# Optimization experiments

Measured on AMD Instinct MI355X. Metric: run time of the kernel, lower is better.

The kernel has to match this reference:

```python
import jax, jax.numpy as jnp
import numpy as np

B, S, FDIM = 8, 512, 512
SUB = 4
DIM = FDIM // SUB            # 128 (reformer model dim)
HEADS, LOCAL_HEADS = 8, 2
LSH_HEADS = HEADS - LOCAL_HEADS
DH = 64                      # dim_head
INNER = HEADS * DH           # 512
BUCKET = 64
N_HASHES = 4
MEM = 128                    # num_mem_kv
DEPTH = 2                    # cfg.selfatn.num_layers
T = S * SUB + MEM            # 2176 internal seq (tokens + mem kv)
NB = T // BUCKET             # 34 buckets (even)
WINDOW = BUCKET * 2          # local attention window = 128
SELF_VAL = -5e4              # TOKEN_SELF_ATTN_VALUE
NEG = -1e9


def _ln(x, g, b, eps=1e-5):
    m = jnp.mean(x, -1, keepdims=True)
    v = jnp.mean((x - m) ** 2, -1, keepdims=True)
    return (x - m) * jax.lax.rsqrt(v + eps) * g + b


def _pos_encoding(s, d):
    pos = jnp.arange(s, dtype=jnp.float32)[:, None]
    i = jnp.arange(d, dtype=jnp.float32)
    div = 10000.0 ** (2.0 * i / d)
    pe = jnp.zeros((s, d), jnp.float32)
    pe = pe.at[:, 0::2].set(jnp.sin(pos / div[0::2]))
    pe = pe.at[:, 1::2].set(jnp.cos(pos / div[1::2]))
    return pe


def _l2norm(x, eps=1e-12):
    n = jnp.linalg.norm(x, axis=-1, keepdims=True)
    return x / jnp.maximum(n, eps)


def _lsh_attn(qk, v, rot):
    # qk, v: [Bh, T, DH]; rot: [DH, N_HASHES, NB//2] random rotations
    Bh, t, d = qk.shape
    rv = jnp.einsum('btf,fhi->bhti', qk, rot)
    rv = jnp.concatenate([rv, -rv], axis=-1)               # [Bh, nh, t, NB]
    buckets = jnp.argmax(rv, axis=-1)
    buckets = buckets + (jnp.arange(N_HASHES) * NB)[None, :, None]
    buckets = buckets.reshape(Bh, N_HASHES * t)
    ticker = jnp.arange(N_HASHES * t) % t
    key = buckets * t + ticker                             # sort by (bucket, pos)
    perm = jnp.argsort(key, axis=-1)                       # stable
    undo = jnp.argsort(perm, axis=-1)
    st = perm % t                                          # source positions
    sqk = jnp.take_along_axis(qk, st[..., None], axis=1)
    sv = jnp.take_along_axis(v, st[..., None], axis=1)
    C = N_HASHES * NB
    bq_t = st.reshape(Bh, C, BUCKET)
    bq = sqk.reshape(Bh, C, BUCKET, d)
    bv = sv.reshape(Bh, C, BUCKET, d)
    bk = _l2norm(bq)                                       # shared-QK: normalized keys
    look = lambda x: jnp.concatenate([x, jnp.roll(x, 1, axis=1)], axis=2)
    bk, bv, bkv_t = look(bk), look(bv), look(bq_t)
    dots = jnp.einsum('bcie,bcje->bcij', bq, bk) * (d ** -0.5)
    dots = jnp.where(bq_t[..., None] < bkv_t[:, :, None, :], NEG, dots)      # causal
    dots = jnp.where(bq_t[..., None] == bkv_t[:, :, None, :], SELF_VAL, dots)  # self
    lse = jax.nn.logsumexp(dots, axis=-1, keepdims=True)
    bo = jnp.einsum('bcij,bcje->bcie', jnp.exp(dots - lse), bv)
    so = bo.reshape(Bh, N_HASHES * t, d)
    slog = lse.reshape(Bh, N_HASHES * t)
    o = jnp.take_along_axis(so, undo[..., None], axis=1).reshape(Bh, N_HASHES, t, d)
    logits = jnp.take_along_axis(slog, undo, axis=1).reshape(Bh, N_HASHES, t, 1)
    w = jnp.exp(logits - jax.nn.logsumexp(logits, axis=1, keepdims=True))
    return (o * w).sum(axis=1)


def _local_attn(q, v):
    # shared-QK causal local attention, look_backward=1; q, v: [Bh, T, DH]
    Bh, t, d = q.shape
    W = t // WINDOW
    k = _l2norm(q)
    bq = q.reshape(Bh, W, WINDOW, d)
    bk = k.reshape(Bh, W, WINDOW, d)
    bv = v.reshape(Bh, W, WINDOW, d)
    tt = jnp.arange(t).reshape(W, WINDOW)
    prev = lambda x: jnp.concatenate([jnp.zeros_like(x[:, :1]), x[:, :-1]], axis=1)
    bk2 = jnp.concatenate([prev(bk), bk], axis=2)          # [Bh, W, 2W, d]
    bv2 = jnp.concatenate([prev(bv), bv], axis=2)
    tprev = jnp.concatenate([jnp.full((1, WINDOW), -1), tt[:-1]], axis=0)
    bkv_t = jnp.concatenate([tprev, tt], axis=1)           # [W, 2*WINDOW]
    dots = jnp.einsum('bwie,bwje->bwij', bq, bk2) * (d ** -0.5)
    dots = jnp.where(tt[:, :, None] == bkv_t[:, None, :], SELF_VAL, dots)
    dots = jnp.where(tt[:, :, None] < bkv_t[:, None, :], NEG, dots)
    dots = jnp.where((bkv_t == -1)[:, None, :], NEG, dots)
    attn = jax.nn.softmax(dots, axis=-1)
    return jnp.einsum('bwij,bwje->bwie', attn, bv2).reshape(Bh, t, d)


def _attn_layer(x, w_qk, w_v, mem_kv, w_out, b_out, rot):
    b, t0, _ = x.shape
    mem = jnp.broadcast_to(mem_kv, (b, MEM, DIM))
    xm = jnp.concatenate([x, mem], axis=1)                 # [b, T, DIM]
    qk = (xm @ w_qk).reshape(b, T, HEADS, DH).transpose(0, 2, 1, 3)
    v = (xm @ w_v).reshape(b, T, HEADS, DH).transpose(0, 2, 1, 3)
    merge = lambda a: a.reshape(-1, T, DH)
    out_loc = _local_attn(merge(qk[:, :LOCAL_HEADS]), merge(v[:, :LOCAL_HEADS]))
    out_lsh = _lsh_attn(merge(qk[:, LOCAL_HEADS:]), merge(v[:, LOCAL_HEADS:]), rot)
    out = jnp.concatenate([out_loc.reshape(b, LOCAL_HEADS, T, DH),
                           out_lsh.reshape(b, LSH_HEADS, T, DH)], axis=1)
    out = out.transpose(0, 2, 1, 3).reshape(b, T, INNER)
    return out[:, :t0] @ w_out + b_out


def setup_inputs() -> dict:
    key = jax.random.key(0)
    ks = jax.random.split(key, 20)
    std = 0.01  # init_network truncated-normal std
    p = lambda k, sh: std * jax.random.truncated_normal(k, -2.0, 2.0, sh, jnp.float32)
    return {
        'features': jax.random.normal(ks[0], (B, S, FDIM), jnp.float32),
        'w_qk': p(ks[1], (DEPTH, DIM, INNER)),
        'w_v': p(ks[2], (DEPTH, DIM, INNER)),
        'mem_kv': p(ks[3], (DEPTH, MEM, DIM)),
        'w_out': p(ks[4], (DEPTH, INNER, DIM)),
        'b_out': p(ks[5], (DEPTH, DIM)),
        'ln1_g': jnp.ones((DEPTH, DIM), jnp.float32),
        'ln1_b': jnp.zeros((DEPTH, DIM), jnp.float32),
        'ff_w1': p(ks[6], (DEPTH, DIM, 4 * DIM)),
        'ff_b1': p(ks[7], (DEPTH, 4 * DIM)),
        'ff_w2': p(ks[8], (DEPTH, 4 * DIM, DIM)),
        'ff_b2': p(ks[9], (DEPTH, DIM)),
        'ln2_g': jnp.ones((DEPTH, DIM), jnp.float32),
        'ln2_b': jnp.zeros((DEPTH, DIM), jnp.float32),
        'lnf_g': jnp.ones((DIM,), jnp.float32),
        'lnf_b': jnp.zeros((DIM,), jnp.float32),
        'rotations': jax.random.normal(ks[10], (DEPTH, DH, N_HASHES, NB // 2), jnp.float32),
    }


def reference(features, w_qk, w_v, mem_kv, w_out, b_out, ln1_g, ln1_b,
              ff_w1, ff_b1, ff_w2, ff_b2, ln2_g, ln2_b, lnf_g, lnf_b, rotations):
    b, s, fd = features.shape
    x = features + _pos_encoding(s, fd)                    # PositionalEncoding
    x = x.reshape(b, s * SUB, fd // SUB)                   # subspace split
    # reversible Reformer blocks: y1 = x1 + attn(ln(x2)); y2 = x2 + ff(ln(y1))
    x1, x2 = x, x
    for i in range(DEPTH):
        a_in = _ln(x2, ln1_g[i], ln1_b[i])
        y1 = x1 + _attn_layer(a_in, w_qk[i], w_v[i], mem_kv[i], w_out[i], b_out[i], rotations[i])
        g_in = _ln(y1, ln2_g[i], ln2_b[i])
        h = jax.nn.gelu(g_in @ ff_w1[i] + ff_b1[i], approximate=False)
        y2 = x2 + (h @ ff_w2[i] + ff_b2[i])
        x1, x2 = y1, y2
    x = 0.5 * (x1 + x2)                                    # mean of the two streams
    x = _ln(x, lnf_g, lnf_b)                               # final norm
    x = x.reshape(b, s, fd)                                # merge subspaces back
    return x.mean(axis=1)                                  # AvgPool
```

## Files before the change

kernel.cpp:

```cpp
#include <hip/hip_runtime.h>
#include <math.h>

#define NB_ 34
#define NEGV  (-1e9f)
#define SELFV (-5e4f)

typedef __attribute__((ext_vector_type(8))) short short8;
typedef __attribute__((ext_vector_type(4))) float floatx4;

__device__ __forceinline__ unsigned short f2bf(float f) {
  unsigned int u = __float_as_uint(f);
  u += 0x7fffu + ((u >> 16) & 1u);
  return (unsigned short)(u >> 16);
}
__device__ __forceinline__ float bflo(unsigned int u) { return __uint_as_float(u << 16); }
__device__ __forceinline__ float bfhi(unsigned int u) { return __uint_as_float(u & 0xffff0000u); }

__device__ __forceinline__ void load_row64_bf(const unsigned short* __restrict__ p, float* q) {
#pragma unroll
  for (int k = 0; k < 8; ++k) {
    uint4 u = ((const uint4*)p)[k];
    q[8*k+0]=bflo(u.x); q[8*k+1]=bfhi(u.x);
    q[8*k+2]=bflo(u.y); q[8*k+3]=bfhi(u.y);
    q[8*k+4]=bflo(u.z); q[8*k+5]=bfhi(u.z);
    q[8*k+6]=bflo(u.w); q[8*k+7]=bfhi(u.w);
  }
}


__global__ void pos_kernel(const float* __restrict__ feat, float* __restrict__ x1,
                           float* __restrict__ x2) {
  int idx = blockIdx.x*256 + threadIdx.x;
  int d = idx & 127, t = (idx >> 7) & 2047, b = idx >> 18;
  int s = t >> 2, c = ((t & 3) << 7) | d;
  float div = powf(10000.0f, (float)c * (1.0f/256.0f));
  float arg = (float)s / div;
  float pe = (c & 1) ? cosf(arg) : sinf(arg);
  float val = feat[((size_t)b*512 + s)*512 + c] + pe;
  x1[idx] = val; x2[idx] = val;
}

__global__ __launch_bounds__(256) void ln_kernel(
    const float* __restrict__ in, const float* __restrict__ in2,
    const float* __restrict__ g, const float* __restrict__ bta,
    void* __restrict__ out, int rows, int ou, int oa, int obf) {
  int wid = threadIdx.x >> 6, lane = threadIdx.x & 63;
  int row = blockIdx.x*4 + wid;
  if (row >= rows) return;
  float2 x = ((const float2*)(in + (size_t)row*128))[lane];
  if (in2) {
    float2 y = ((const float2*)(in2 + (size_t)row*128))[lane];
    x.x = 0.5f*(x.x + y.x); x.y = 0.5f*(x.y + y.y);
  }
  float s = x.x + x.y;
#pragma unroll
  for (int m = 1; m < 64; m <<= 1) s += __shfl_xor(s, m, 64);
  float mean = s * (1.0f/128.0f);
  float dx = x.x - mean, dy = x.y - mean;
  float v = dx*dx + dy*dy;
#pragma unroll
  for (int m = 1; m < 64; m <<= 1) v += __shfl_xor(v, m, 64);
  float inv = 1.0f / sqrtf(v*(1.0f/128.0f) + 1e-5f);
  int orow = (ou == oa) ? row : (row/ou)*oa + (row%ou);
  float2 gg = ((const float2*)g)[lane];
  float2 bb = ((const float2*)bta)[lane];
  float ox = dx*inv*gg.x + bb.x, oy = dy*inv*gg.y + bb.y;
  if (obf) {
    ((unsigned int*)out)[(size_t)orow*64 + lane] =
        (unsigned int)f2bf(ox) | ((unsigned int)f2bf(oy) << 16);
  } else {
    float2 o; o.x = ox; o.y = oy;
    ((float2*)((float*)out + (size_t)orow*128))[lane] = o;
  }
}

__global__ void memfill_kernel(const float* __restrict__ mem,
                               unsigned short* __restrict__ xmb) {
  int idx = blockIdx.x*256 + threadIdx.x;
  int d = idx & 127, r = (idx >> 7) & 127, b = idx >> 14;
  xmb[((size_t)b*2176 + 2048 + r)*128 + d] = f2bf(mem[(r << 7) | d]);
}

__global__ void wconv_kernel(const float* __restrict__ w, unsigned short* __restrict__ wt,
                             int K, int N) {
  int idx = blockIdx.x*256 + threadIdx.x;
  int k = idx % K, n = idx / K;
  wt[idx] = f2bf(w[(size_t)k*N + n]);
}

__global__ __launch_bounds__(256) void gemm_bf16(
    const unsigned short* __restrict__ A, const unsigned short* __restrict__ Wt,
    const float* __restrict__ bias, const float* __restrict__ resid,
    float* __restrict__ C, unsigned short* __restrict__ Cb,
    int M, int N, int K, int au, int aa, int act) {
  __shared__ __align__(16) unsigned short As[64*40];
  __shared__ __align__(16) unsigned short Bs[64*40];
  int tid = threadIdx.x;
  int wid = tid >> 6, l15 = tid & 15, quad = (tid & 63) >> 4;
  int mb = blockIdx.y, nb = blockIdx.x;
  int r = tid >> 2, cc = (tid & 3)*8;
  int rg = mb*64 + r;
  int rp = (au == aa) ? rg : (rg/au)*aa + (rg%au);
  const unsigned short* arow = A + (size_t)rp*K + cc;
  const unsigned short* brow = Wt + (size_t)(nb*64 + r)*K + cc;
  floatx4 acc[4];
#pragma unroll
  for (int mt = 0; mt < 4; ++mt) acc[mt] = (floatx4){0.f,0.f,0.f,0.f};
  for (int k0 = 0; k0 < K; k0 += 32) {
    *(short8*)&As[r*40 + cc] = *(const short8*)(arow + k0);
    *(short8*)&Bs[r*40 + cc] = *(const short8*)(brow + k0);
    __syncthreads();
    short8 bfr = *(const short8*)&Bs[(wid*16 + l15)*40 + quad*8];
#pragma unroll
    for (int mt = 0; mt < 4; ++mt) {
      short8 afr = *(const short8*)&As[(mt*16 + l15)*40 + quad*8];
      acc[mt] = __builtin_amdgcn_mfma_f32_16x16x32_bf16(afr, bfr, acc[mt], 0, 0, 0);
    }
    __syncthreads();
  }
  int n = nb*64 + wid*16 + l15;
  float bi = bias ? bias[n] : 0.f;
#pragma unroll
  for (int mt = 0; mt < 4; ++mt) {
#pragma unroll
    for (int rr = 0; rr < 4; ++rr) {
      int m = mb*64 + mt*16 + quad*4 + rr;
      float val = acc[mt][rr] + bi;
      if (act) val = 0.5f*val*(1.0f + erff(val*0.70710678118654752f));
      if (resid) val += resid[(size_t)m*N + n];
      if (Cb) Cb[(size_t)m*N + n] = f2bf(val);
      else    C[(size_t)m*N + n] = val;
    }
  }
}

__global__ __launch_bounds__(256) void gemm_qv(
    const unsigned short* __restrict__ A, const unsigned short* __restrict__ Wt,
    unsigned short* __restrict__ Q, unsigned short* __restrict__ V) {
  __shared__ __align__(16) unsigned short As[64*40];
  __shared__ __align__(16) unsigned short Bs[64*40];
  int tid = threadIdx.x;
  int wid = tid >> 6, l15 = tid & 15, quad = (tid & 63) >> 4;
  int mb = blockIdx.y, nb = blockIdx.x;
  int r = tid >> 2, cc = (tid & 3)*8;
  const unsigned short* arow = A + (size_t)(mb*64 + r)*128 + cc;
  const unsigned short* brow = Wt + (size_t)(nb*64 + r)*128 + cc;
  floatx4 acc[4];
#pragma unroll
  for (int mt = 0; mt < 4; ++mt) acc[mt] = (floatx4){0.f,0.f,0.f,0.f};
#pragma unroll
  for (int k0 = 0; k0 < 128; k0 += 32) {
    *(short8*)&As[r*40 + cc] = *(const short8*)(arow + k0);
    *(short8*)&Bs[r*40 + cc] = *(const short8*)(brow + k0);
    __syncthreads();
    short8 bfr = *(const short8*)&Bs[(wid*16 + l15)*40 + quad*8];
#pragma unroll
    for (int mt = 0; mt < 4; ++mt) {
      short8 afr = *(const short8*)&As[(mt*16 + l15)*40 + quad*8];
      acc[mt] = __builtin_amdgcn_mfma_f32_16x16x32_bf16(afr, bfr, acc[mt], 0, 0, 0);
    }
    __syncthreads();
  }
  int n = nb*64 + wid*16 + l15;
#pragma unroll
  for (int mt = 0; mt < 4; ++mt) {
#pragma unroll
    for (int rr = 0; rr < 4; ++rr) {
      int m = mb*64 + mt*16 + quad*4 + rr;
      unsigned short bv = f2bf(acc[mt][rr]);
      if (n < 512) Q[(size_t)m*512 + n] = bv;
      else         V[(size_t)m*512 + (n - 512)] = bv;
    }
  }
}

__global__ __launch_bounds__(256) void norm_kernel(const unsigned short* __restrict__ qkb,
                                                   float* __restrict__ nrm) {
  int idx = blockIdx.x*256 + threadIdx.x;
  int head = idx & 7, row = idx >> 3;
  const uint4* src = (const uint4*)(qkb + (size_t)row*512 + head*64);
  float ss = 0.f;
#pragma unroll
  for (int k = 0; k < 8; ++k) {
    uint4 u = src[k];
    ss += bflo(u.x)*bflo(u.x) + bfhi(u.x)*bfhi(u.x)
        + bflo(u.y)*bflo(u.y) + bfhi(u.y)*bfhi(u.y)
        + bflo(u.z)*bflo(u.z) + bfhi(u.z)*bfhi(u.z)
        + bflo(u.w)*bflo(u.w) + bfhi(u.w)*bfhi(u.w);
  }
  int b = row / 2176, t = row % 2176;
  nrm[((size_t)b*8 + head)*2176 + t] = 1.0f / fmaxf(sqrtf(ss), 1e-12f);
}

__global__ __launch_bounds__(128) void local_attn_mfma(
    const unsigned short* __restrict__ qkb, const unsigned short* __restrict__ vbb,
    const float* __restrict__ nrm,
    unsigned short* __restrict__ opart, float* __restrict__ lpart) {
  __shared__ __align__(16) unsigned short qq[128*72];
  __shared__ __align__(16) unsigned short kk[128*72];
  __shared__ __align__(16) unsigned short vt[64*136];
  __shared__ __align__(16) unsigned short ptile[2][16*136];
  __shared__ float invn[128];

  int blk = blockIdx.x;
  int part = blk & 1;
  int bw = blk >> 1;
  int bh = bw / 17, w = bw % 17;
  int b = bh >> 1, coloff = (bh & 1)*64;
  int tid = threadIdx.x;
  int t_qbase = w*128;

  unsigned short* obase = opart + (size_t)(part*16 + bh)*2176*64;
  float* lbase = lpart + (size_t)(part*16 + bh)*2176;

  if (part == 0 && w == 0) {
    uint4 z = {0,0,0,0};
    uint4* orow = (uint4*)(obase + (size_t)tid*64);
#pragma unroll
    for (int j = 0; j < 8; ++j) orow[j] = z;
    lbase[tid] = -1e9f;
    return;
  }

  int tkbase = part ? t_qbase : (t_qbase - 128);
  const float* nrmh = nrm + ((size_t)b*8 + (bh & 1))*2176;
  invn[tid] = nrmh[tkbase + tid];

  {
    const unsigned short* qr = qkb + ((size_t)(b*2176 + t_qbase + tid)*512 + coloff);
#pragma unroll
    for (int k = 0; k < 8; ++k) *(uint4*)&qq[tid*72 + k*8] = ((const uint4*)qr)[k];
  }
  if (part == 0) {
    const unsigned short* qr = qkb + ((size_t)(b*2176 + t_qbase - 128 + tid)*512 + coloff);
#pragma unroll
    for (int k = 0; k < 8; ++k) *(uint4*)&kk[tid*72 + k*8] = ((const uint4*)qr)[k];
  }
  if (tid < 64) {
    const unsigned short* vrA = vbb + ((size_t)(b*2176 + tkbase + 2*tid)*512 + coloff);
    const unsigned short* vrB = vrA + 512;
    unsigned int* vt32 = (unsigned int*)vt;
#pragma unroll
    for (int k = 0; k < 8; ++k) {
      uint4 ua = ((const uint4*)vrA)[k];
      uint4 uc = ((const uint4*)vrB)[k];
      const unsigned short* pa = (const unsigned short*)&ua;
      const unsigned short* pc = (const unsigned short*)&uc;
#pragma unroll
      for (int j = 0; j < 8; ++j) {
        int d = 8*k + j;
        vt32[d*68 + tid] = (unsigned int)pa[j] | ((unsigned int)pc[j] << 16);
      }
    }
  }
  __syncthreads();

  int wid = tid >> 6, l15 = tid & 15, quad = (tid & 63) >> 4;
  const unsigned short* keyrows = part ? qq : kk;
  float sm8[8];
#pragma unroll
  for (int nt = 0; nt < 8; ++nt) sm8[nt] = invn[nt*16 + l15] * 0.125f;
  int qrow0 = wid*64;
  unsigned short* pt = &ptile[wid][0];

#pragma unroll
  for (int mt = 0; mt < 4; ++mt) {
    floatx4 acc[8];
#pragma unroll
    for (int nt = 0; nt < 8; ++nt) acc[nt] = (floatx4){0.f,0.f,0.f,0.f};
#pragma unroll
    for (int ks = 0; ks < 2; ++ks) {
      short8 afr = *(const short8*)&qq[(qrow0 + mt*16 + l15)*72 + ks*32 + quad*8];
#pragma unroll
      for (int nt = 0; nt < 8; ++nt) {
        short8 bfr = *(const short8*)&keyrows[(nt*16 + l15)*72 + ks*32 + quad*8];
        acc[nt] = __builtin_amdgcn_mfma_f32_16x16x32_bf16(afr, bfr, acc[nt], 0, 0, 0);
      }
    }
    float invl[4];
#pragma unroll
    for (int r = 0; r < 4; ++r) {
      int row = qrow0 + mt*16 + quad*4 + r;
      int t_q = t_qbase + row;
      float sv[8]; float mx = -INFINITY;
#pragma unroll
      for (int nt = 0; nt < 8; ++nt) {
        float sc = acc[nt][r] * sm8[nt];
        int t_k = tkbase + nt*16 + l15;
        sc = (t_k > t_q) ? NEGV : (t_k == t_q ? SELFV : sc);
        sv[nt] = sc; mx = fmaxf(mx, sc);
      }
#pragma unroll
      for (int m2 = 1; m2 < 16; m2 <<= 1) mx = fmaxf(mx, __shfl_xor(mx, m2, 64));
      float l = 0.f;
#pragma unroll
      for (int nt = 0; nt < 8; ++nt) { float pe = expf(sv[nt] - mx); sv[nt] = pe; l += pe; }
#pragma unroll
      for (int m2 = 1; m2 < 16; m2 <<= 1) l += __shfl_xor(l, m2, 64);
      invl[r] = 1.0f / l;
#pragma unroll
      for (int nt = 0; nt < 8; ++nt)
        pt[(quad*4 + r)*136 + nt*16 + l15] = f2bf(sv[nt]);
      if (l15 == 0) lbase[t_q] = mx + logf(l);
    }
#pragma unroll
    for (int nt = 0; nt < 4; ++nt) {
      floatx4 po = (floatx4){0.f,0.f,0.f,0.f};
#pragma unroll
      for (int ks = 0; ks < 4; ++ks) {
        short8 afr = *(const short8*)&pt[l15*136 + ks*32 + quad*8];
        short8 bfr = *(const short8*)&vt[(nt*16 + l15)*136 + ks*32 + quad*8];
        po = __builtin_amdgcn_mfma_f32_16x16x32_bf16(afr, bfr, po, 0, 0, 0);
      }
      int d = nt*16 + l15;
#pragma unroll
      for (int r = 0; r < 4; ++r) {
        int t_q = t_qbase + qrow0 + mt*16 + quad*4 + r;
        obase[(size_t)t_q*64 + d] = f2bf(po[r] * invl[r]);
      }
    }
  }
}

__global__ void local_comb(const unsigned short* __restrict__ opart,
                           const float* __restrict__ lpart,
                           unsigned short* __restrict__ aob) {
  int idx = blockIdx.x*256 + threadIdx.x;
  if (idx >= 16*2176*8) return;
  int f8 = idx & 7;
  int p  = (idx >> 3) % 2176;
  int bh = idx / (8*2176);
  float lg0 = lpart[(size_t)bh*2176 + p];
  float lg1 = lpart[(size_t)(16 + bh)*2176 + p];
  float m = fmaxf(lg0, lg1);
  float e0 = expf(lg0 - m), e1 = expf(lg1 - m);
  float inv = 1.0f / (e0 + e1);
  float w0 = e0*inv, w1 = e1*inv;
  uint4 u0 = ((const uint4*)(opart + ((size_t)bh*2176 + p)*64))[f8];
  uint4 u1 = ((const uint4*)(opart + ((size_t)(16 + bh)*2176 + p)*64))[f8];
  uint4 o;
  o.x = (unsigned int)f2bf(w0*bflo(u0.x) + w1*bflo(u1.x)) |
        ((unsigned int)f2bf(w0*bfhi(u0.x) + w1*bfhi(u1.x)) << 16);
  o.y = (unsigned int)f2bf(w0*bflo(u0.y) + w1*bflo(u1.y)) |
        ((unsigned int)f2bf(w0*bfhi(u0.y) + w1*bfhi(u1.y)) << 16);
  o.z = (unsigned int)f2bf(w0*bflo(u0.z) + w1*bflo(u1.z)) |
        ((unsigned int)f2bf(w0*bfhi(u0.z) + w1*bfhi(u1.z)) << 16);
  o.w = (unsigned int)f2bf(w0*bflo(u0.w) + w1*bflo(u1.w)) |
        ((unsigned int)f2bf(w0*bfhi(u0.w) + w1*bfhi(u1.w)) << 16);
  int b = bh >> 1;
  ((uint4*)(aob + ((size_t)(b*2176 + p)*512 + (bh & 1)*64 + f8*8)))[0] = o;
}

__global__ __launch_bounds__(256) void hash_kernel(
    const unsigned short* __restrict__ qkb, const float* __restrict__ rot,
    int* __restrict__ bucket) {
  __shared__ float rl[64*68];
  for (int l = threadIdx.x; l < 4352; l += 256) rl[l] = rot[l];
  __syncthreads();
  int idx = blockIdx.x*256 + threadIdx.x;
  int p = idx % 2176, bh = idx / 2176;
  int b = bh / 6, hh = bh % 6;
  float q[64];
  load_row64_bf(qkb + ((size_t)(b*2176 + p)*512 + (2+hh)*64), q);
  for (int h = 0; h < 4; ++h) {
    float rv[17];
#pragma unroll
    for (int k = 0; k < 17; ++k) rv[k] = 0.f;
    for (int d = 0; d < 64; ++d) {
      float qd = q[d];
      const float* rp = &rl[d*68 + h*17];
#pragma unroll
      for (int k = 0; k < 17; ++k) rv[k] = fmaf(qd, rp[k], rv[k]);
    }
    float best = rv[0]; int bi = 0;
#pragma unroll
    for (int k = 1; k < 34; ++k) {
      float val = (k < 17) ? rv[k] : -rv[k-17];
      if (val > best) { best = val; bi = k; }
    }
    bucket[(size_t)(bh*4 + h)*2176 + p] = bi;
  }
}

__global__ __launch_bounds__(256) void sort_kernel(const int* __restrict__ bucket,
                                                   int* __restrict__ st) {
  __shared__ int sb[2176];
  __shared__ int cnt[NB_*256];
  __shared__ int csum[256];
  int tid = threadIdx.x;
  int bhh = blockIdx.x;
  const int* bin = bucket + (size_t)bhh*2176;
  for (int p = tid; p < 2176; p += 256) sb[p] = bin[p];
#pragma unroll
  for (int j = 0; j < NB_; ++j) cnt[j*256 + tid] = 0;
  __syncthreads();
  int s0 = tid*9;
  int e = s0 + 9; if (e > 2176) e = 2176;
  for (int p = s0; p < e; ++p) cnt[sb[p]*256 + tid] += 1;
  __syncthreads();
  {
    int sum = 0;
    int base0 = tid*NB_;
#pragma unroll
    for (int j = 0; j < NB_; ++j) {
      int v = cnt[base0 + j];
      cnt[base0 + j] = sum;
      sum += v;
    }
    csum[tid] = sum;
  }
  __syncthreads();
  for (int off = 1; off < 256; off <<= 1) {
    int v = (tid >= off) ? csum[tid - off] : 0;
    __syncthreads();
    csum[tid] += v;
    __syncthreads();
  }
  {
    int base = tid ? csum[tid-1] : 0;
    int base0 = tid*NB_;
#pragma unroll
    for (int j = 0; j < NB_; ++j) cnt[base0 + j] += base;
  }
  __syncthreads();
  int bh = bhh >> 2, h = bhh & 3;
  int* outp = st + (size_t)bh*8704 + h*2176;
  for (int p = s0; p < e; ++p) {
    int bk = sb[p];
    int r = cnt[bk*256 + tid]++;
    outp[r] = p;
  }
}

__global__ __launch_bounds__(128) void lsh_attn_mfma(
    const unsigned short* __restrict__ qkb, const unsigned short* __restrict__ vbb,
    const float* __restrict__ nrm, const int* __restrict__ st,
    unsigned short* __restrict__ o_all, float* __restrict__ logits) {
  __shared__ __align__(16) unsigned short qq[192*72];
  __shared__ __align__(16) unsigned short vt[64*200];
  __shared__ __align__(16) unsigned short ptile[2][16*136];
  __shared__ int   tkl[192];
  __shared__ float invn[192];

  int blk = blockIdx.x;
  int bh = blk / 68, pair = blk % 68;
  int c0 = pair*2;
  int b = bh / 6, coloff = (2 + bh % 6)*64;
  int tid = threadIdx.x;
  const float* nrmh = nrm + ((size_t)b*8 + 2 + bh % 6)*2176;

#pragma unroll
  for (int rr = 0; rr < 2; ++rr) {
    if (rr == 1 && tid >= 64) break;
    int r = (rr == 0) ? tid : 128 + tid;
    int cr = c0 - 1 + (r >> 6); if (cr < 0) cr += 136;
    int p = st[(size_t)bh*8704 + cr*64 + (r & 63)];
    tkl[r] = p;
    invn[r] = nrmh[p];
    const unsigned short* qr = qkb + ((size_t)(b*2176 + p)*512 + coloff);
#pragma unroll
    for (int k = 0; k < 8; ++k) *(uint4*)&qq[r*72 + k*8] = ((const uint4*)qr)[k];
  }
  if (tid < 96) {
    int r0 = 2*tid, r1 = r0 + 1;
    int cr0 = c0 - 1 + (r0 >> 6); if (cr0 < 0) cr0 += 136;
    int cr1 = c0 - 1 + (r1 >> 6); if (cr1 < 0) cr1 += 136;
    int p0 = st[(size_t)bh*8704 + cr0*64 + (r0 & 63)];
    int p1 = st[(size_t)bh*8704 + cr1*64 + (r1 & 63)];
    const unsigned short* a = vbb + ((size_t)(b*2176 + p0)*512 + coloff);
    const unsigned short* c = vbb + ((size_t)(b*2176 + p1)*512 + coloff);
    unsigned int* vt32 = (unsigned int*)vt;
#pragma unroll
    for (int k = 0; k < 8; ++k) {
      uint4 ua = ((const uint4*)a)[k];
      uint4 uc = ((const uint4*)c)[k];
      const unsigned short* pa = (const unsigned short*)&ua;
      const unsigned short* pc = (const unsigned short*)&uc;
#pragma unroll
      for (int j = 0; j < 8; ++j) {
        int d = 8*k + j;
        vt32[d*100 + tid] = (unsigned int)pa[j] | ((unsigned int)pc[j] << 16);
      }
    }
  }
  __syncthreads();

  int wid = tid >> 6, l15 = tid & 15, quad = (tid & 63) >> 4;
  int kbase = wid*64, qbase = 64 + wid*64;
  int c = c0 + wid;
  int h = c / NB_;
  float sm8[8]; int tk8[8];
#pragma unroll
  for (int nt = 0; nt < 8; ++nt) {
    int kr = kbase + nt*16 + l15;
    sm8[nt] = invn[kr] * 0.125f;
    tk8[nt] = tkl[kr];
  }
  float* logrow = logits + (size_t)(bh*4 + h)*2176;
  unsigned short* obase = o_all + (size_t)(bh*4 + h)*2176*64;
  unsigned short* pt = &ptile[wid][0];

#pragma unroll
  for (int mt = 0; mt < 4; ++mt) {
    floatx4 acc[8];
#pragma unroll
    for (int nt = 0; nt < 8; ++nt) acc[nt] = (floatx4){0.f,0.f,0.f,0.f};
#pragma unroll
    for (int ks = 0; ks < 2; ++ks) {
      short8 afr = *(const short8*)&qq[(qbase + mt*16 + l15)*72 + ks*32 + quad*8];
#pragma unroll
      for (int nt = 0; nt < 8; ++nt) {
        short8 bfr = *(const short8*)&qq[(kbase + nt*16 + l15)*72 + ks*32 + quad*8];
        acc[nt] = __builtin_amdgcn_mfma_f32_16x16x32_bf16(afr, bfr, acc[nt], 0, 0, 0);
      }
    }
    float invl[4];
#pragma unroll
    for (int r = 0; r < 4; ++r) {
      int t_q = tkl[qbase + mt*16 + quad*4 + r];
      float sv8[8]; float mx = -INFINITY;
#pragma unroll
      for (int nt = 0; nt < 8; ++nt) {
        float sc = acc[nt][r] * sm8[nt];
        int t_k = tk8[nt];
        sc = (t_k > t_q) ? NEGV : (t_k == t_q ? SELFV : sc);
        sv8[nt] = sc; mx = fmaxf(mx, sc);
      }
#pragma unroll
      for (int m2 = 1; m2 < 16; m2 <<= 1) mx = fmaxf(mx, __shfl_xor(mx, m2, 64));
      float l = 0.f;
#pragma unroll
      for (int nt = 0; nt < 8; ++nt) { float pe = expf(sv8[nt] - mx); sv8[nt] = pe; l += pe; }
#pragma unroll
      for (int m2 = 1; m2 < 16; m2 <<= 1) l += __shfl_xor(l, m2, 64);
      invl[r] = 1.0f / l;
#pragma unroll
      for (int nt = 0; nt < 8; ++nt)
        pt[(quad*4 + r)*136 + nt*16 + l15] = f2bf(sv8[nt]);
      if (l15 == 0) logrow[t_q] = mx + logf(l);
    }
#pragma unroll
    for (int nt = 0; nt < 4; ++nt) {
      floatx4 po = (floatx4){0.f,0.f,0.f,0.f};
#pragma unroll
      for (int ks = 0; ks < 4; ++ks) {
        short8 afr = *(const short8*)&pt[l15*136 + ks*32 + quad*8];
        short8 bfr = *(const short8*)&vt[(nt*16 + l15)*200 + kbase + ks*32 + quad*8];
        po = __builtin_amdgcn_mfma_f32_16x16x32_bf16(afr, bfr, po, 0, 0, 0);
      }
      int d = nt*16 + l15;
#pragma unroll
      for (int r = 0; r < 4; ++r) {
        int p_q = tkl[qbase + mt*16 + quad*4 + r];
        obase[(size_t)p_q*64 + d] = f2bf(po[r] * invl[r]);
      }
    }
  }
}

__global__ void comb_kernel(const unsigned short* __restrict__ o_all,
                            const float* __restrict__ logits,
                            unsigned short* __restrict__ aob) {
  int idx = blockIdx.x*256 + threadIdx.x;
  int f8 = idx & 7;
  int p  = (idx >> 3) % 2176;
  int bh = idx / (8*2176);
  float lg0 = logits[(size_t)(bh*4+0)*2176 + p];
  float lg1 = logits[(size_t)(bh*4+1)*2176 + p];
  float lg2 = logits[(size_t)(bh*4+2)*2176 + p];
  float lg3 = logits[(size_t)(bh*4+3)*2176 + p];
  float m = fmaxf(fmaxf(lg0, lg1), fmaxf(lg2, lg3));
  float e0 = expf(lg0-m), e1 = expf(lg1-m), e2 = expf(lg2-m), e3 = expf(lg3-m);
  float inv = 1.0f / (e0+e1+e2+e3);
  float wh[4] = {e0*inv, e1*inv, e2*inv, e3*inv};
  float o[8];
#pragma unroll
  for (int d = 0; d < 8; ++d) o[d] = 0.f;
#pragma unroll
  for (int h = 0; h < 4; ++h) {
    float wg = wh[h];
    uint4 u = ((const uint4*)(o_all + ((size_t)(bh*4+h)*2176 + p)*64))[f8];
    o[0] = fmaf(wg, bflo(u.x), o[0]); o[1] = fmaf(wg, bfhi(u.x), o[1]);
    o[2] = fmaf(wg, bflo(u.y), o[2]); o[3] = fmaf(wg, bfhi(u.y), o[3]);
    o[4] = fmaf(wg, bflo(u.z), o[4]); o[5] = fmaf(wg, bfhi(u.z), o[5]);
    o[6] = fmaf(wg, bflo(u.w), o[6]); o[7] = fmaf(wg, bfhi(u.w), o[7]);
  }
  int b = bh / 6, hh = bh % 6;
  uint4 u;
  u.x = (unsigned int)f2bf(o[0]) | ((unsigned int)f2bf(o[1]) << 16);
  u.y = (unsigned int)f2bf(o[2]) | ((unsigned int)f2bf(o[3]) << 16);
  u.z = (unsigned int)f2bf(o[4]) | ((unsigned int)f2bf(o[5]) << 16);
  u.w = (unsigned int)f2bf(o[6]) | ((unsigned int)f2bf(o[7]) << 16);
  ((uint4*)(aob + ((size_t)(b*2176 + p)*512 + (2+hh)*64 + f8*8)))[0] = u;
}

__global__ __launch_bounds__(256) void pool_kernel(const float* __restrict__ xln,
                                                   float* __restrict__ out) {
  int o = blockIdx.x*4 + (threadIdx.x >> 6);
  int lane = threadIdx.x & 63;
  int c = o & 511, b = o >> 9;
  int sub = c >> 7, d = c & 127;
  const float* p = xln + ((size_t)b*2048 + sub)*128 + d;
  float s = 0.f;
#pragma unroll
  for (int j = 0; j < 8; ++j) s += p[(size_t)(lane + 64*j)*512];
#pragma unroll
  for (int m = 1; m < 64; m <<= 1) s += __shfl_xor(s, m, 64);
  if (lane == 0) out[o] = s * (1.0f/512.0f);
}

#define OFF_X1    0ull
#define OFF_X2    2097152ull
#define OFF_XM    4194304ull
#define OFF_XMB   6422528ull
#define OFF_QKB   7536640ull
#define OFF_VB    16449536ull
#define OFF_AOB   25362432ull
#define OFF_OALL  29818880ull
#define OFF_LOG   43188224ull
#define OFF_BKT   43606016ull
#define OFF_ST    44023808ull
#define OFF_WTB   44441600ull
#define OFF_NRM   44769280ull
#define WS_FLOATS 44908544ull

extern "C" void kernel_launch(void* const* d_in, const int* in_sizes, int n_in,
                              void* d_out, int out_size, void* d_ws, size_t ws_size,
                              hipStream_t stream) {
  (void)in_sizes; (void)n_in; (void)out_size;
  if (ws_size < WS_FLOATS * 4ull) return;

  const float* feat  = (const float*)d_in[0];
  const float* w_qk  = (const float*)d_in[1];
  const float* w_v   = (const float*)d_in[2];
  const float* memkv = (const float*)d_in[3];
  const float* w_out = (const float*)d_in[4];
  const float* b_out = (const float*)d_in[5];
  const float* ln1g  = (const float*)d_in[6];
  const float* ln1b  = (const float*)d_in[7];
  const float* ffw1  = (const float*)d_in[8];
  const float* ffb1  = (const float*)d_in[9];
  const float* ffw2  = (const float*)d_in[10];
  const float* ffb2  = (const float*)d_in[11];
  const float* ln2g  = (const float*)d_in[12];
  const float* ln2b  = (const float*)d_in[13];
  const float* lnfg  = (const float*)d_in[14];
  const float* lnfb  = (const float*)d_in[15];
  const float* rots  = (const float*)d_in[16];

  float* ws = (float*)d_ws;
  float* x1   = ws + OFF_X1;
  float* x2   = ws + OFF_X2;
  float* xm   = ws + OFF_XM;
  unsigned short* xmb = (unsigned short*)(ws + OFF_XMB);
  unsigned short* qkb = (unsigned short*)(ws + OFF_QKB);
  unsigned short* vbb = (unsigned short*)(ws + OFF_VB);
  unsigned short* aob = (unsigned short*)(ws + OFF_AOB);
  unsigned short* hb  = (unsigned short*)(ws + OFF_AOB);
  unsigned short* oall = (unsigned short*)(ws + OFF_OALL);
  unsigned short* opart = (unsigned short*)(ws + OFF_OALL);
  float* lpart = ws + OFF_OALL + 2228224ull;
  float* logi = ws + OFF_LOG;
  int*   bkt  = (int*)(ws + OFF_BKT);
  int*   st   = (int*)(ws + OFF_ST);
  unsigned short* wtb = (unsigned short*)(ws + OFF_WTB);
  float* nrm  = ws + OFF_NRM;
  float* outp = (float*)d_out;

  pos_kernel<<<8192, 256, 0, stream>>>(feat, x1, x2);

  for (int i = 0; i < 2; ++i) {
    wconv_kernel<<<256, 256, 0, stream>>>(w_qk + i*65536, wtb + (i*5+0)*65536, 128, 512);
    wconv_kernel<<<256, 256, 0, stream>>>(w_v  + i*65536, wtb + (i*5+1)*65536, 128, 512);
    wconv_kernel<<<256, 256, 0, stream>>>(w_out+ i*65536, wtb + (i*5+2)*65536, 512, 128);
    wconv_kernel<<<256, 256, 0, stream>>>(ffw1 + i*65536, wtb + (i*5+3)*65536, 128, 512);
    wconv_kernel<<<256, 256, 0, stream>>>(ffw2 + i*65536, wtb + (i*5+4)*65536, 512, 128);
  }

  for (int i = 0; i < 2; ++i) {
    const unsigned short* Wqv = wtb + (i*5+0)*65536;
    const unsigned short* Wo  = wtb + (i*5+2)*65536;
    const unsigned short* W1  = wtb + (i*5+3)*65536;
    const unsigned short* W2  = wtb + (i*5+4)*65536;

    ln_kernel<<<4096, 256, 0, stream>>>(x2, nullptr, ln1g + i*128, ln1b + i*128,
                                        xmb, 16384, 2048, 2176, 1);
    memfill_kernel<<<512, 256, 0, stream>>>(memkv + i*16384, xmb);

    gemm_qv<<<dim3(16, 272), 256, 0, stream>>>(xmb, Wqv, qkb, vbb);
    norm_kernel<<<544, 256, 0, stream>>>(qkb, nrm);

    local_attn_mfma<<<544, 128, 0, stream>>>(qkb, vbb, nrm, opart, lpart);
    local_comb<<<1088, 256, 0, stream>>>(opart, lpart, aob);

    hash_kernel<<<408, 256, 0, stream>>>(qkb, rots + i*4352, bkt);
    sort_kernel<<<192, 256, 0, stream>>>(bkt, st);
    lsh_attn_mfma<<<3264, 128, 0, stream>>>(qkb, vbb, nrm, st, oall, logi);
    comb_kernel<<<3264, 256, 0, stream>>>(oall, logi, aob);

    gemm_bf16<<<dim3(2, 256), 256, 0, stream>>>(aob, Wo, b_out + i*128, x1, x1, nullptr,
                                                16384, 128, 512, 2048, 2176, 0);
    ln_kernel<<<4096, 256, 0, stream>>>(x1, nullptr, ln2g + i*128, ln2b + i*128,
                                        xmb, 16384, 1, 1, 1);
    gemm_bf16<<<dim3(8, 256), 256, 0, stream>>>(xmb, W1, ffb1 + i*512, nullptr, nullptr, hb,
                                                16384, 512, 128, 1, 1, 1);
    gemm_bf16<<<dim3(2, 256), 256, 0, stream>>>(hb, W2, ffb2 + i*128, x2, x2, nullptr,
                                                16384, 128, 512, 1, 1, 0);
  }

  ln_kernel<<<4096, 256, 0, stream>>>(x1, x2, lnfg, lnfb, xm, 16384, 1, 1, 0);
  pool_kernel<<<1024, 256, 0, stream>>>(xm, outp);
}
```

Measured before the change: 763.3 us.

## Fuse local and LSH attention launches, combine kernels, memfill, and weight conversion

Merges the local-window and LSH attention kernels into one launch that branches on block index, and merges their two combine kernels into one. The memory-kv fill is folded into the first layernorm launch, and the ten weight-conversion launches become one. The local partial outputs get their own workspace region so both attention paths can run at the same time. This cuts launch count and lets the two attention workloads fill the GPU together, but it uses a larger shared-memory allocation per block, which may lower occupancy for the local path.

After: 704.3 us. 1.08x faster.

```diff
diff --git a/kernel.cpp b/kernel.cpp
--- a/kernel.cpp
+++ b/kernel.cpp
@@ -43,10 +43,20 @@
 __global__ __launch_bounds__(256) void ln_kernel(
     const float* __restrict__ in, const float* __restrict__ in2,
     const float* __restrict__ g, const float* __restrict__ bta,
-    void* __restrict__ out, int rows, int ou, int oa, int obf) {
+    void* __restrict__ out, int rows, int ou, int oa, int obf,
+    const float* __restrict__ mem, int memrows) {
   int wid = threadIdx.x >> 6, lane = threadIdx.x & 63;
   int row = blockIdx.x*4 + wid;
-  if (row >= rows) return;
+  if (row >= rows) {
+    int mr = row - rows;
+    if (!mem || mr >= memrows) return;
+    int bb = mr >> 7, r = mr & 127;
+    int orow2 = bb*2176 + 2048 + r;
+    float2 mv = ((const float2*)(mem + (size_t)r*128))[lane];
+    ((unsigned int*)out)[(size_t)orow2*64 + lane] =
+        (unsigned int)f2bf(mv.x) | ((unsigned int)f2bf(mv.y) << 16);
+    return;
+  }
   float2 x = ((const float2*)(in + (size_t)row*128))[lane];
   if (in2) {
     float2 y = ((const float2*)(in2 + (size_t)row*128))[lane];
@@ -74,18 +84,24 @@
   }
 }
 
-__global__ void memfill_kernel(const float* __restrict__ mem,
-                               unsigned short* __restrict__ xmb) {
+__global__ void wconv_all(const float* __restrict__ w_qk, const float* __restrict__ w_v,
+                          const float* __restrict__ w_out, const float* __restrict__ ffw1,
+                          const float* __restrict__ ffw2, unsigned short* __restrict__ wt) {
   int idx = blockIdx.x*256 + threadIdx.x;
-  int d = idx & 127, r = (idx >> 7) & 127, b = idx >> 14;
-  xmb[((size_t)b*2176 + 2048 + r)*128 + d] = f2bf(mem[(r << 7) | d]);
-}
-
-__global__ void wconv_kernel(const float* __restrict__ w, unsigned short* __restrict__ wt,
-                             int K, int N) {
-  int idx = blockIdx.x*256 + threadIdx.x;
-  int k = idx % K, n = idx / K;
-  wt[idx] = f2bf(w[(size_t)k*N + n]);
+  int m = idx >> 16, j = idx & 65535;
+  int i = m / 5, t = m % 5;
+  const float* src; int K;
+  switch (t) {
+    case 0: src = w_qk; K = 128; break;
+    case 1: src = w_v;  K = 128; break;
+    case 2: src = w_out;K = 512; break;
+    case 3: src = ffw1; K = 128; break;
+    default:src = ffw2; K = 512; break;
+  }
+  src += (size_t)i*65536;
+  int N = 65536 / K;
+  int k = j % K, n = j / K;
+  wt[(size_t)m*65536 + j] = f2bf(src[(size_t)k*N + n]);
 }
 
 __global__ __launch_bounds__(256) void gemm_bf16(
@@ -192,163 +208,262 @@
   nrm[((size_t)b*8 + head)*2176 + t] = 1.0f / fmaxf(sqrtf(ss), 1e-12f);
 }
 
-__global__ __launch_bounds__(128) void local_attn_mfma(
+__global__ __launch_bounds__(128) void fused_attn(
     const unsigned short* __restrict__ qkb, const unsigned short* __restrict__ vbb,
-    const float* __restrict__ nrm,
+    const float* __restrict__ nrm, const int* __restrict__ st,
+    unsigned short* __restrict__ o_all, float* __restrict__ logits,
     unsigned short* __restrict__ opart, float* __restrict__ lpart) {
-  __shared__ __align__(16) unsigned short qq[128*72];
-  __shared__ __align__(16) unsigned short kk[128*72];
-  __shared__ __align__(16) unsigned short vt[64*136];
-  __shared__ __align__(16) unsigned short ptile[2][16*136];
-  __shared__ float invn[128];
-
-  int blk = blockIdx.x;
-  int part = blk & 1;
-  int bw = blk >> 1;
-  int bh = bw / 17, w = bw % 17;
-  int b = bh >> 1, coloff = (bh & 1)*64;
+  __shared__ __align__(16) unsigned char shraw[63488];
   int tid = threadIdx.x;
-  int t_qbase = w*128;
-
-  unsigned short* obase = opart + (size_t)(part*16 + bh)*2176*64;
-  float* lbase = lpart + (size_t)(part*16 + bh)*2176;
-
-  if (part == 0 && w == 0) {
-    uint4 z = {0,0,0,0};
-    uint4* orow = (uint4*)(obase + (size_t)tid*64);
-#pragma unroll
-    for (int j = 0; j < 8; ++j) orow[j] = z;
-    lbase[tid] = -1e9f;
+
+  if (blockIdx.x < 3264) {
+    unsigned short* qq = (unsigned short*)shraw;
+    unsigned short* vt = (unsigned short*)(shraw + 27648);
+    unsigned short* ptile = (unsigned short*)(shraw + 53248);
+    int*   tkl  = (int*)(shraw + 61952);
+    float* invn = (float*)(shraw + 62720);
+
+    int blk = blockIdx.x;
+    int bh = blk / 68, pair = blk % 68;
+    int c0 = pair*2;
+    int b = bh / 6, coloff = (2 + bh % 6)*64;
+    const float* nrmh = nrm + ((size_t)b*8 + 2 + bh % 6)*2176;
+
+#pragma unroll
+    for (int rr = 0; rr < 2; ++rr) {
+      if (rr == 1 && tid >= 64) break;
+      int r = (rr == 0) ? tid : 128 + tid;
+      int cr = c0 - 1 + (r >> 6); if (cr < 0) cr += 136;
+      int p = st[(size_t)bh*8704 + cr*64 + (r & 63)];
+      tkl[r] = p;
+      invn[r] = nrmh[p];
+      const unsigned short* qr = qkb + ((size_t)(b*2176 + p)*512 + coloff);
+#pragma unroll
+      for (int k = 0; k < 8; ++k) *(uint4*)&qq[r*72 + k*8] = ((const uint4*)qr)[k];
+    }
+    if (tid < 96) {
+      int r0 = 2*tid, r1 = r0 + 1;
+      int cr0 = c0 - 1 + (r0 >> 6); if (cr0 < 0) cr0 += 136;
+      int cr1 = c0 - 1 + (r1 >> 6); if (cr1 < 0) cr1 += 136;
+      int p0 = st[(size_t)bh*8704 + cr0*64 + (r0 & 63)];
+      int p1 = st[(size_t)bh*8704 + cr1*64 + (r1 & 63)];
+      const unsigned short* a = vbb + ((size_t)(b*2176 + p0)*512 + coloff);
+      const unsigned short* c = vbb + ((size_t)(b*2176 + p1)*512 + coloff);
+      unsigned int* vt32 = (unsigned int*)vt;
+#pragma unroll
+      for (int k = 0; k < 8; ++k) {
+        uint4 ua = ((const uint4*)a)[k];
+        uint4 uc = ((const uint4*)c)[k];
+        const unsigned short* pa = (const unsigned short*)&ua;
+        const unsigned short* pc = (const unsigned short*)&uc;
+#pragma unroll
+        for (int j = 0; j < 8; ++j) {
+          int d = 8*k + j;
+          vt32[d*100 + tid] = (unsigned int)pa[j] | ((unsigned int)pc[j] << 16);
+        }
+      }
+    }
+    __syncthreads();
+
+    int wid = tid >> 6, l15 = tid & 15, quad = (tid & 63) >> 4;
+    int kbase = wid*64, qbase = 64 + wid*64;
+    int c = c0 + wid;
+    int h = c / NB_;
+    float sm8[8]; int tk8[8];
+#pragma unroll
+    for (int nt = 0; nt < 8; ++nt) {
+      int kr = kbase + nt*16 + l15;
+      sm8[nt] = invn[kr] * 0.125f;
+      tk8[nt] = tkl[kr];
+    }
+    float* logrow = logits + (size_t)(bh*4 + h)*2176;
+    unsigned short* obase = o_all + (size_t)(bh*4 + h)*2176*64;
+    unsigned short* pt = ptile + wid*(16*136);
+
+#pragma unroll
+    for (int mt = 0; mt < 4; ++mt) {
+      floatx4 acc[8];
+#pragma unroll
+      for (int nt = 0; nt < 8; ++nt) acc[nt] = (floatx4){0.f,0.f,0.f,0.f};
+#pragma unroll
+      for (int ks = 0; ks < 2; ++ks) {
+        short8 afr = *(const short8*)&qq[(qbase + mt*16 + l15)*72 + ks*32 + quad*8];
+#pragma unroll
+        for (int nt = 0; nt < 8; ++nt) {
+          short8 bfr = *(const short8*)&qq[(kbase + nt*16 + l15)*72 + ks*32 + quad*8];
+          acc[nt] = __builtin_amdgcn_mfma_f32_16x16x32_bf16(afr, bfr, acc[nt], 0, 0, 0);
+        }
+      }
+      float invl[4];
+#pragma unroll
+      for (int r = 0; r < 4; ++r) {
+        int t_q = tkl[qbase + mt*16 + quad*4 + r];
+        float sv8[8]; float mx = -INFINITY;
+#pragma unroll
+        for (int nt = 0; nt < 8; ++nt) {
+          float sc = acc[nt][r] * sm8[nt];
+          int t_k = tk8[nt];
+          sc = (t_k > t_q) ? NEGV : (t_k == t_q ? SELFV : sc);
+          sv8[nt] = sc; mx = fmaxf(mx, sc);
+        }
+#pragma unroll
+        for (int m2 = 1; m2 < 16; m2 <<= 1) mx = fmaxf(mx, __shfl_xor(mx, m2, 64));
+        float l = 0.f;
+#pragma unroll
+        for (int nt = 0; nt < 8; ++nt) { float pe = expf(sv8[nt] - mx); sv8[nt] = pe; l += pe; }
+#pragma unroll
+        for (int m2 = 1; m2 < 16; m2 <<= 1) l += __shfl_xor(l, m2, 64);
+        invl[r] = 1.0f / l;
+#pragma unroll
+        for (int nt = 0; nt < 8; ++nt)
+          pt[(quad*4 + r)*136 + nt*16 + l15] = f2bf(sv8[nt]);
+        if (l15 == 0) logrow[t_q] = mx + logf(l);
+      }
+#pragma unroll
+      for (int nt = 0; nt < 4; ++nt) {
+        floatx4 po = (floatx4){0.f,0.f,0.f,0.f};
+#pragma unroll
+        for (int ks = 0; ks < 4; ++ks) {
+          short8 afr = *(const short8*)&pt[l15*136 + ks*32 + quad*8];
+          short8 bfr = *(const short8*)&vt[(nt*16 + l15)*200 + kbase + ks*32 + quad*8];
+          po = __builtin_amdgcn_mfma_f32_16x16x32_bf16(afr, bfr, po, 0, 0, 0);
+        }
+        int d = nt*16 + l15;
+#pragma unroll
+        for (int r = 0; r < 4; ++r) {
+          int p_q = tkl[qbase + mt*16 + quad*4 + r];
+          obase[(size_t)p_q*64 + d] = f2bf(po[r] * invl[r]);
+        }
+      }
+    }
     return;
   }
 
-  int tkbase = part ? t_qbase : (t_qbase - 128);
-  const float* nrmh = nrm + ((size_t)b*8 + (bh & 1))*2176;
-  invn[tid] = nrmh[tkbase + tid];
-
   {
-    const unsigned short* qr = qkb + ((size_t)(b*2176 + t_qbase + tid)*512 + coloff);
-#pragma unroll
-    for (int k = 0; k < 8; ++k) *(uint4*)&qq[tid*72 + k*8] = ((const uint4*)qr)[k];
-  }
-  if (part == 0) {
-    const unsigned short* qr = qkb + ((size_t)(b*2176 + t_qbase - 128 + tid)*512 + coloff);
-#pragma unroll
-    for (int k = 0; k < 8; ++k) *(uint4*)&kk[tid*72 + k*8] = ((const uint4*)qr)[k];
-  }
-  if (tid < 64) {
-    const unsigned short* vrA = vbb + ((size_t)(b*2176 + tkbase + 2*tid)*512 + coloff);
-    const unsigned short* vrB = vrA + 512;
-    unsigned int* vt32 = (unsigned int*)vt;
-#pragma unroll
-    for (int k = 0; k < 8; ++k) {
-      uint4 ua = ((const uint4*)vrA)[k];
-      uint4 uc = ((const uint4*)vrB)[k];
-      const unsigned short* pa = (const unsigned short*)&ua;
-      const unsigned short* pc = (const unsigned short*)&uc;
-#pragma unroll
-      for (int j = 0; j < 8; ++j) {
-        int d = 8*k + j;
-        vt32[d*68 + tid] = (unsigned int)pa[j] | ((unsigned int)pc[j] << 16);
+    unsigned short* qq = (unsigned short*)shraw;
+    unsigned short* kk = (unsigned short*)(shraw + 18432);
+    unsigned short* vt = (unsigned short*)(shraw + 36864);
+    unsigned short* ptile = (unsigned short*)(shraw + 54272);
+    float* invn = (float*)(shraw + 62976);
+
+    int blk = blockIdx.x - 3264;
+    int part = blk & 1;
+    int bw = blk >> 1;
+    int bh = bw / 17, w = bw % 17;
+    int b = bh >> 1, coloff = (bh & 1)*64;
+    int t_qbase = w*128;
+
+    unsigned short* obase = opart + (size_t)(part*16 + bh)*2176*64;
+    float* lbase = lpart + (size_t)(part*16 + bh)*2176;
+
+    if (part == 0 && w == 0) {
+      uint4 z = {0,0,0,0};
+      uint4* orow = (uint4*)(obase + (size_t)tid*64);
+#pragma unroll
+      for (int j = 0; j < 8; ++j) orow[j] = z;
+      lbase[tid] = -1e9f;
+      return;
+    }
+
+    int tkbase = part ? t_qbase : (t_qbase - 128);
+    const float* nrmh = nrm + ((size_t)b*8 + (bh & 1))*2176;
+    invn[tid] = nrmh[tkbase + tid];
+
+    {
+      const unsigned short* qr = qkb + ((size_t)(b*2176 + t_qbase + tid)*512 + coloff);
+#pragma unroll
+      for (int k = 0; k < 8; ++k) *(uint4*)&qq[tid*72 + k*8] = ((const uint4*)qr)[k];
+    }
+    if (part == 0) {
+      const unsigned short* qr = qkb + ((size_t)(b*2176 + t_qbase - 128 + tid)*512 + coloff);
+#pragma unroll
+      for (int k = 0; k < 8; ++k) *(uint4*)&kk[tid*72 + k*8] = ((const uint4*)qr)[k];
+    }
+    if (tid < 64) {
+      const unsigned short* vrA = vbb + ((size_t)(b*2176 + tkbase + 2*tid)*512 + coloff);
+      const unsigned short* vrB = vrA + 512;
+      unsigned int* vt32 = (unsigned int*)vt;
+#pragma unroll
+      for (int k = 0; k < 8; ++k) {
+        uint4 ua = ((const uint4*)vrA)[k];
+        uint4 uc = ((const uint4*)vrB)[k];
+        const unsigned short* pa = (const unsigned short*)&ua;
+        const unsigned short* pc = (const unsigned short*)&uc;
+#pragma unroll
+        for (int j = 0; j < 8; ++j) {
+          int d = 8*k + j;
+          vt32[d*68 + tid] = (unsigned int)pa[j] | ((unsigned int)pc[j] << 16);
+        }
       }
     }
-  }
-  __syncthreads();
-
-  int wid = tid >> 6, l15 = tid & 15, quad = (tid & 63) >> 4;
-  const unsigned short* keyrows = part ? qq : kk;
-  float sm8[8];
-#pragma unroll
-  for (int nt = 0; nt < 8; ++nt) sm8[nt] = invn[nt*16 + l15] * 0.125f;
-  int qrow0 = wid*64;
-  unsigned short* pt = &ptile[wid][0];
-
-#pragma unroll
-  for (int mt = 0; mt < 4; ++mt) {
-    floatx4 acc[8];
-#pragma unroll
-    for (int nt = 0; nt < 8; ++nt) acc[nt] = (floatx4){0.f,0.f,0.f,0.f};
-#pragma unroll
-    for (int ks = 0; ks < 2; ++ks) {
-      short8 afr = *(const short8*)&qq[(qrow0 + mt*16 + l15)*72 + ks*32 + quad*8];
-#pragma unroll
-      for (int nt = 0; nt < 8; ++nt) {
-        short8 bfr = *(const short8*)&keyrows[(nt*16 + l15)*72 + ks*32 + quad*8];
-        acc[nt] = __builtin_amdgcn_mfma_f32_16x16x32_bf16(afr, bfr, acc[nt], 0, 0, 0);
+    __syncthreads();
+
+    int wid = tid >> 6, l15 = tid & 15, quad = (tid & 63) >> 4;
+    const unsigned short* keyrows = part ? qq : kk;
+    float sm8[8];
+#pragma unroll
+    for (int nt = 0; nt < 8; ++nt) sm8[nt] = invn[nt*16 + l15] * 0.125f;
+    int qrow0 = wid*64;
+    unsigned short* pt = ptile + wid*(16*136);
+
+#pragma unroll
+    for (int mt = 0; mt < 4; ++mt) {
+      floatx4 acc[8];
+#pragma unroll
+      for (int nt = 0; nt < 8; ++nt) acc[nt] = (floatx4){0.f,0.f,0.f,0.f};
+#pragma unroll
+      for (int ks = 0; ks < 2; ++ks) {
+        short8 afr = *(const short8*)&qq[(qrow0 + mt*16 + l15)*72 + ks*32 + quad*8];
+#pragma unroll
+        for (int nt = 0; nt < 8; ++nt) {
+          short8 bfr = *(const short8*)&keyrows[(nt*16 + l15)*72 + ks*32 + quad*8];
+          acc[nt] = __builtin_amdgcn_mfma_f32_16x16x32_bf16(afr, bfr, acc[nt], 0, 0, 0);
+        }
       }
-    }
-    float invl[4];
-#pragma unroll
-    for (int r = 0; r < 4; ++r) {
-      int row = qrow0 + mt*16 + quad*4 + r;
-      int t_q = t_qbase + row;
-      float sv[8]; float mx = -INFINITY;
-#pragma unroll
-      for (int nt = 0; nt < 8; ++nt) {
-        float sc = acc[nt][r] * sm8[nt];
-        int t_k = tkbase + nt*16 + l15;
-        sc = (t_k > t_q) ? NEGV : (t_k == t_q ? SELFV : sc);
-        sv[nt] = sc; mx = fmaxf(mx, sc);
+      float invl[4];
+#pragma unroll
+      for (int r = 0; r < 4; ++r) {
+        int row = qrow0 + mt*16 + quad*4 + r;
+        int t_q = t_qbase + row;
+        float sv[8]; float mx = -INFINITY;
+#pragma unroll
+        for (int nt = 0; nt < 8; ++nt) {
+          float sc = acc[nt][r] * sm8[nt];
+          int t_k = tkbase + nt*16 + l15;
+          sc = (t_k > t_q) ? NEGV : (t_k == t_q ? SELFV : sc);
+          sv[nt] = sc; mx = fmaxf(mx, sc);
+        }
+#pragma unroll
+        for (int m2 = 1; m2 < 16; m2 <<= 1) mx = fmaxf(mx, __shfl_xor(mx, m2, 64));
+        float l = 0.f;
+#pragma unroll
+        for (int nt = 0; nt < 8; ++nt) { float pe = expf(sv[nt] - mx); sv[nt] = pe; l += pe; }
+#pragma unroll
+        for (int m2 = 1; m2 < 16; m2 <<= 1) l += __shfl_xor(l, m2, 64);
+        invl[r] = 1.0f / l;
+#pragma unroll
+        for (int nt = 0; nt < 8; ++nt)
+          pt[(quad*4 + r)*136 + nt*16 + l15] = f2bf(sv[nt]);
+        if (l15 == 0) lbase[t_q] = mx + logf(l);
       }
 #pragma unroll
-      for (int m2 = 1; m2 < 16; m2 <<= 1) mx = fmaxf(mx, __shfl_xor(mx, m2, 64));
-      float l = 0.f;
-#pragma unroll
-      for (int nt = 0; nt < 8; ++nt) { float pe = expf(sv[nt] - mx); sv[nt] = pe; l += pe; }
-#pragma unroll
-      for (int m2 = 1; m2 < 16; m2 <<= 1) l += __shfl_xor(l, m2, 64);
-      invl[r] = 1.0f / l;
-#pragma unroll
-      for (int nt = 0; nt < 8; ++nt)
-        pt[(quad*4 + r)*136 + nt*16 + l15] = f2bf(sv[nt]);
-      if (l15 == 0) lbase[t_q] = mx + logf(l);
-    }
-#pragma unroll
-    for (int nt = 0; nt < 4; ++nt) {
-      floatx4 po = (floatx4){0.f,0.f,0.f,0.f};
-#pragma unroll
-      for (int ks = 0; ks < 4; ++ks) {
-        short8 afr = *(const short8*)&pt[l15*136 + ks*32 + quad*8];
-        short8 bfr = *(const short8*)&vt[(nt*16 + l15)*136 + ks*32 + quad*8];
-        po = __builtin_amdgcn_mfma_f32_16x16x32_bf16(afr, bfr, po, 0, 0, 0);
+      for (int nt = 0; nt < 4; ++nt) {
+        floatx4 po = (floatx4){0.f,0.f,0.f,0.f};
+#pragma unroll
+        for (int ks = 0; ks < 4; ++ks) {
+          short8 afr = *(const short8*)&pt[l15*136 + ks*32 + quad*8];
+          short8 bfr = *(const short8*)&vt[(nt*16 + l15)*136 + ks*32 + quad*8];
+          po = __builtin_amdgcn_mfma_f32_16x16x32_bf16(afr, bfr, po, 0, 0, 0);
+        }
+        int d = nt*16 + l15;
+#pragma unroll
+        for (int r = 0; r < 4; ++r) {
+          int t_q = t_qbase + qrow0 + mt*16 + quad*4 + r;
+          obase[(size_t)t_q*64 + d] = f2bf(po[r] * invl[r]);
+        }
       }
-      int d = nt*16 + l15;
-#pragma unroll
-      for (int r = 0; r < 4; ++r) {
-        int t_q = t_qbase + qrow0 + mt*16 + quad*4 + r;
-        obase[(size_t)t_q*64 + d] = f2bf(po[r] * invl[r]);
-      }
-    }
-  }
-}
-
-__global__ void local_comb(const unsigned short* __restrict__ opart,
-                           const float* __restrict__ lpart,
-                           unsigned short* __restrict__ aob) {
-  int idx = blockIdx.x*256 + threadIdx.x;
-  if (idx >= 16*2176*8) return;
-  int f8 = idx & 7;
-  int p  = (idx >> 3) % 2176;
-  int bh = idx / (8*2176);
-  float lg0 = lpart[(size_t)bh*2176 + p];
-  float lg1 = lpart[(size_t)(16 + bh)*2176 + p];
-  float m = fmaxf(lg0, lg1);
-  float e0 = expf(lg0 - m), e1 = expf(lg1 - m);
-  float inv = 1.0f / (e0 + e1);
-  float w0 = e0*inv, w1 = e1*inv;
-  uint4 u0 = ((const uint4*)(opart + ((size_t)bh*2176 + p)*64))[f8];
-  uint4 u1 = ((const uint4*)(opart + ((size_t)(16 + bh)*2176 + p)*64))[f8];
-  uint4 o;
-  o.x = (unsigned int)f2bf(w0*bflo(u0.x) + w1*bflo(u1.x)) |
-        ((unsigned int)f2bf(w0*bfhi(u0.x) + w1*bfhi(u1.x)) << 16);
-  o.y = (unsigned int)f2bf(w0*bflo(u0.y) + w1*bflo(u1.y)) |
-        ((unsigned int)f2bf(w0*bfhi(u0.y) + w1*bfhi(u1.y)) << 16);
-  o.z = (unsigned int)f2bf(w0*bflo(u0.z) + w1*bflo(u1.z)) |
-        ((unsigned int)f2bf(w0*bfhi(u0.z) + w1*bfhi(u1.z)) << 16);
-  o.w = (unsigned int)f2bf(w0*bflo(u0.w) + w1*bflo(u1.w)) |
-        ((unsigned int)f2bf(w0*bfhi(u0.w) + w1*bfhi(u1.w)) << 16);
-  int b = bh >> 1;
-  ((uint4*)(aob + ((size_t)(b*2176 + p)*512 + (bh & 1)*64 + f8*8)))[0] = o;
+    }
+  }
 }
 
 __global__ __launch_bounds__(256) void hash_kernel(
@@ -432,166 +547,68 @@
   }
 }
 
-__global__ __launch_bounds__(128) void lsh_attn_mfma(
-    const unsigned short* __restrict__ qkb, const unsigned short* __restrict__ vbb,
-    const float* __restrict__ nrm, const int* __restrict__ st,
-    unsigned short* __restrict__ o_all, float* __restrict__ logits) {
-  __shared__ __align__(16) unsigned short qq[192*72];
-  __shared__ __align__(16) unsigned short vt[64*200];
-  __shared__ __align__(16) unsigned short ptile[2][16*136];
-  __shared__ int   tkl[192];
-  __shared__ float invn[192];
-
-  int blk = blockIdx.x;
-  int bh = blk / 68, pair = blk % 68;
-  int c0 = pair*2;
-  int b = bh / 6, coloff = (2 + bh % 6)*64;
-  int tid = threadIdx.x;
-  const float* nrmh = nrm + ((size_t)b*8 + 2 + bh % 6)*2176;
-
-#pragma unroll
-  for (int rr = 0; rr < 2; ++rr) {
-    if (rr == 1 && tid >= 64) break;
-    int r = (rr == 0) ? tid : 128 + tid;
-    int cr = c0 - 1 + (r >> 6); if (cr < 0) cr += 136;
-    int p = st[(size_t)bh*8704 + cr*64 + (r & 63)];
-    tkl[r] = p;
-    invn[r] = nrmh[p];
-    const unsigned short* qr = qkb + ((size_t)(b*2176 + p)*512 + coloff);
-#pragma unroll
-    for (int k = 0; k < 8; ++k) *(uint4*)&qq[r*72 + k*8] = ((const uint4*)qr)[k];
-  }
-  if (tid < 96) {
-    int r0 = 2*tid, r1 = r0 + 1;
-    int cr0 = c0 - 1 + (r0 >> 6); if (cr0 < 0) cr0 += 136;
-    int cr1 = c0 - 1 + (r1 >> 6); if (cr1 < 0) cr1 += 136;
-    int p0 = st[(size_t)bh*8704 + cr0*64 + (r0 & 63)];
-    int p1 = st[(size_t)bh*8704 + cr1*64 + (r1 & 63)];
-    const unsigned short* a = vbb + ((size_t)(b*2176 + p0)*512 + coloff);
-    const unsigned short* c = vbb + ((size_t)(b*2176 + p1)*512 + coloff);
-    unsigned int* vt32 = (unsigned int*)vt;
-#pragma unroll
-    for (int k = 0; k < 8; ++k) {
-      uint4 ua = ((const uint4*)a)[k];
-      uint4 uc = ((const uint4*)c)[k];
-      const unsigned short* pa = (const unsigned short*)&ua;
-      const unsigned short* pc = (const unsigned short*)&uc;
-#pragma unroll
-      for (int j = 0; j < 8; ++j) {
-        int d = 8*k + j;
-        vt32[d*100 + tid] = (unsigned int)pa[j] | ((unsigned int)pc[j] << 16);
-      }
-    }
-  }
-  __syncthreads();
-
-  int wid = tid >> 6, l15 = tid & 15, quad = (tid & 63) >> 4;
-  int kbase = wid*64, qbase = 64 + wid*64;
-  int c = c0 + wid;
-  int h = c / NB_;
-  float sm8[8]; int tk8[8];
-#pragma unroll
-  for (int nt = 0; nt < 8; ++nt) {
-    int kr = kbase + nt*16 + l15;
-    sm8[nt] = invn[kr] * 0.125f;
-    tk8[nt] = tkl[kr];
-  }
-  float* logrow = logits + (size_t)(bh*4 + h)*2176;
-  unsigned short* obase = o_all + (size_t)(bh*4 + h)*2176*64;
-  unsigned short* pt = &ptile[wid][0];
-
-#pragma unroll
-  for (int mt = 0; mt < 4; ++mt) {
-    floatx4 acc[8];
-#pragma unroll
-    for (int nt = 0; nt < 8; ++nt) acc[nt] = (floatx4){0.f,0.f,0.f,0.f};
-#pragma unroll
-    for (int ks = 0; ks < 2; ++ks) {
-      short8 afr = *(const short8*)&qq[(qbase + mt*16 + l15)*72 + ks*32 + quad*8];
-#pragma unroll
-      for (int nt = 0; nt < 8; ++nt) {
-        short8 bfr = *(const short8*)&qq[(kbase + nt*16 + l15)*72 + ks*32 + quad*8];
-        acc[nt] = __builtin_amdgcn_mfma_f32_16x16x32_bf16(afr, bfr, acc[nt], 0, 0, 0);
-      }
-    }
-    float invl[4];
-#pragma unroll
-    for (int r = 0; r < 4; ++r) {
-      int t_q = tkl[qbase + mt*16 + quad*4 + r];
-      float sv8[8]; float mx = -INFINITY;
-#pragma unroll
-      for (int nt = 0; nt < 8; ++nt) {
-        float sc = acc[nt][r] * sm8[nt];
-        int t_k = tk8[nt];
-        sc = (t_k > t_q) ? NEGV : (t_k == t_q ? SELFV : sc);
-        sv8[nt] = sc; mx = fmaxf(mx, sc);
-      }
-#pragma unroll
-      for (int m2 = 1; m2 < 16; m2 <<= 1) mx = fmaxf(mx, __shfl_xor(mx, m2, 64));
-      float l = 0.f;
-#pragma unroll
-      for (int nt = 0; nt < 8; ++nt) { float pe = expf(sv8[nt] - mx); sv8[nt] = pe; l += pe; }
-#pragma unroll
-      for (int m2 = 1; m2 < 16; m2 <<= 1) l += __shfl_xor(l, m2, 64);
-      invl[r] = 1.0f / l;
-#pragma unroll
-      for (int nt = 0; nt < 8; ++nt)
-        pt[(quad*4 + r)*136 + nt*16 + l15] = f2bf(sv8[nt]);
-      if (l15 == 0) logrow[t_q] = mx + logf(l);
-    }
-#pragma unroll
-    for (int nt = 0; nt < 4; ++nt) {
-      floatx4 po = (floatx4){0.f,0.f,0.f,0.f};
-#pragma unroll
-      for (int ks = 0; ks < 4; ++ks) {
-        short8 afr = *(const short8*)&pt[l15*136 + ks*32 + quad*8];
-        short8 bfr = *(const short8*)&vt[(nt*16 + l15)*200 + kbase + ks*32 + quad*8];
-        po = __builtin_amdgcn_mfma_f32_16x16x32_bf16(afr, bfr, po, 0, 0, 0);
-      }
-      int d = nt*16 + l15;
-#pragma unroll
-      for (int r = 0; r < 4; ++r) {
-        int p_q = tkl[qbase + mt*16 + quad*4 + r];
-        obase[(size_t)p_q*64 + d] = f2bf(po[r] * invl[r]);
-      }
-    }
-  }
-}
-
-__global__ void comb_kernel(const unsigned short* __restrict__ o_all,
-                            const float* __restrict__ logits,
-                            unsigned short* __restrict__ aob) {
+__global__ void comb_fused(const unsigned short* __restrict__ o_all,
+                           const float* __restrict__ logits,
+                           const unsigned short* __restrict__ opart,
+                           const float* __restrict__ lpart,
+                           unsigned short* __restrict__ aob) {
   int idx = blockIdx.x*256 + threadIdx.x;
-  int f8 = idx & 7;
-  int p  = (idx >> 3) % 2176;
-  int bh = idx / (8*2176);
-  float lg0 = logits[(size_t)(bh*4+0)*2176 + p];
-  float lg1 = logits[(size_t)(bh*4+1)*2176 + p];
-  float lg2 = logits[(size_t)(bh*4+2)*2176 + p];
-  float lg3 = logits[(size_t)(bh*4+3)*2176 + p];
-  float m = fmaxf(fmaxf(lg0, lg1), fmaxf(lg2, lg3));
-  float e0 = expf(lg0-m), e1 = expf(lg1-m), e2 = expf(lg2-m), e3 = expf(lg3-m);
-  float inv = 1.0f / (e0+e1+e2+e3);
-  float wh[4] = {e0*inv, e1*inv, e2*inv, e3*inv};
-  float o[8];
-#pragma unroll
-  for (int d = 0; d < 8; ++d) o[d] = 0.f;
-#pragma unroll
-  for (int h = 0; h < 4; ++h) {
-    float wg = wh[h];
-    uint4 u = ((const uint4*)(o_all + ((size_t)(bh*4+h)*2176 + p)*64))[f8];
-    o[0] = fmaf(wg, bflo(u.x), o[0]); o[1] = fmaf(wg, bfhi(u.x), o[1]);
-    o[2] = fmaf(wg, bflo(u.y), o[2]); o[3] = fmaf(wg, bfhi(u.y), o[3]);
-    o[4] = fmaf(wg, bflo(u.z), o[4]); o[5] = fmaf(wg, bfhi(u.z), o[5]);
-    o[6] = fmaf(wg, bflo(u.w), o[6]); o[7] = fmaf(wg, bfhi(u.w), o[7]);
-  }
-  int b = bh / 6, hh = bh % 6;
-  uint4 u;
-  u.x = (unsigned int)f2bf(o[0]) | ((unsigned int)f2bf(o[1]) << 16);
-  u.y = (unsigned int)f2bf(o[2]) | ((unsigned int)f2bf(o[3]) << 16);
-  u.z = (unsigned int)f2bf(o[4]) | ((unsigned int)f2bf(o[5]) << 16);
-  u.w = (unsigned int)f2bf(o[6]) | ((unsigned int)f2bf(o[7]) << 16);
-  ((uint4*)(aob + ((size_t)(b*2176 + p)*512 + (2+hh)*64 + f8*8)))[0] = u;
+  if (idx < 835584) {
+    int f8 = idx & 7;
+    int p  = (idx >> 3) % 2176;
+    int bh = idx / (8*2176);
+    float lg0 = logits[(size_t)(bh*4+0)*2176 + p];
+    float lg1 = logits[(size_t)(bh*4+1)*2176 + p];
+    float lg2 = logits[(size_t)(bh*4+2)*2176 + p];
+    float lg3 = logits[(size_t)(bh*4+3)*2176 + p];
+    float m = fmaxf(fmaxf(lg0, lg1), fmaxf(lg2, lg3));
+    float e0 = expf(lg0-m), e1 = expf(lg1-m), e2 = expf(lg2-m), e3 = expf(lg3-m);
+    float inv = 1.0f / (e0+e1+e2+e3);
+    float wh[4] = {e0*inv, e1*inv, e2*inv, e3*inv};
+    float o[8];
+#pragma unroll
+    for (int d = 0; d < 8; ++d) o[d] = 0.f;
+#pragma unroll
+    for (int h = 0; h < 4; ++h) {
+      float wg = wh[h];
+      uint4 u = ((const uint4*)(o_all + ((size_t)(bh*4+h)*2176 + p)*64))[f8];
+      o[0] = fmaf(wg, bflo(u.x), o[0]); o[1] = fmaf(wg, bfhi(u.x), o[1]);
+      o[2] = fmaf(wg, bflo(u.y), o[2]); o[3] = fmaf(wg, bfhi(u.y), o[3]);
+      o[4] = fmaf(wg, bflo(u.z), o[4]); o[5] = fmaf(wg, bfhi(u.z), o[5]);
+      o[6] = fmaf(wg, bflo(u.w), o[6]); o[7] = fmaf(wg, bfhi(u.w), o[7]);
+    }
+    int b = bh / 6, hh = bh % 6;
+    uint4 u;
+    u.x = (unsigned int)f2bf(o[0]) | ((unsigned int)f2bf(o[1]) << 16);
+    u.y = (unsigned int)f2bf(o[2]) | ((unsigned int)f2bf(o[3]) << 16);
+    u.z = (unsigned int)f2bf(o[4]) | ((unsigned int)f2bf(o[5]) << 16);
+    u.w = (unsigned int)f2bf(o[6]) | ((unsigned int)f2bf(o[7]) << 16);
+    ((uint4*)(aob + ((size_t)(b*2176 + p)*512 + (2+hh)*64 + f8*8)))[0] = u;
+  } else {
+    int j = idx - 835584;
+    int f8 = j & 7;
+    int p  = (j >> 3) % 2176;
+    int bh = j / (8*2176);
+    float lg0 = lpart[(size_t)bh*2176 + p];
+    float lg1 = lpart[(size_t)(16 + bh)*2176 + p];
+    float m = fmaxf(lg0, lg1);
+    float e0 = expf(lg0 - m), e1 = expf(lg1 - m);
+    float inv = 1.0f / (e0 + e1);
+    float w0 = e0*inv, w1 = e1*inv;
+    uint4 u0 = ((const uint4*)(opart + ((size_t)bh*2176 + p)*64))[f8];
+    uint4 u1 = ((const uint4*)(opart + ((size_t)(16 + bh)*2176 + p)*64))[f8];
+    uint4 o;
+    o.x = (unsigned int)f2bf(w0*bflo(u0.x) + w1*bflo(u1.x)) |
+          ((unsigned int)f2bf(w0*bfhi(u0.x) + w1*bfhi(u1.x)) << 16);
+    o.y = (unsigned int)f2bf(w0*bflo(u0.y) + w1*bflo(u1.y)) |
+          ((unsigned int)f2bf(w0*bfhi(u0.y) + w1*bfhi(u1.y)) << 16);
+    o.z = (unsigned int)f2bf(w0*bflo(u0.z) + w1*bflo(u1.z)) |
+          ((unsigned int)f2bf(w0*bfhi(u0.z) + w1*bfhi(u1.z)) << 16);
+    o.w = (unsigned int)f2bf(w0*bflo(u0.w) + w1*bflo(u1.w)) |
+          ((unsigned int)f2bf(w0*bfhi(u0.w) + w1*bfhi(u1.w)) << 16);
+    int b = bh >> 1;
+    ((uint4*)(aob + ((size_t)(b*2176 + p)*512 + (bh & 1)*64 + f8*8)))[0] = o;
+  }
 }
 
 __global__ __launch_bounds__(256) void pool_kernel(const float* __restrict__ xln,
@@ -622,7 +639,9 @@
 #define OFF_ST    44023808ull
 #define OFF_WTB   44441600ull
 #define OFF_NRM   44769280ull
-#define WS_FLOATS 44908544ull
+#define OFF_OPART 44908544ull
+#define OFF_LPART 47136768ull
+#define WS_FLOATS 47206400ull
 
 extern "C" void kernel_launch(void* const* d_in, const int* in_sizes, int n_in,
                               void* d_out, int out_size, void* d_ws, size_t ws_size,
@@ -658,8 +677,8 @@
   unsigned short* aob = (unsigned short*)(ws + OFF_AOB);
   unsigned short* hb  = (unsigned short*)(ws + OFF_AOB);
   unsigned short* oall = (unsigned short*)(ws + OFF_OALL);
-  unsigned short* opart = (unsigned short*)(ws + OFF_OALL);
-  float* lpart = ws + OFF_OALL + 2228224ull;
+  unsigned short* opart = (unsigned short*)(ws + OFF_OPART);
+  float* lpart = ws + OFF_LPART;
   float* logi = ws + OFF_LOG;
   int*   bkt  = (int*)(ws + OFF_BKT);
   int*   st   = (int*)(ws + OFF_ST);
@@ -668,14 +687,7 @@
   float* outp = (float*)d_out;
 
   pos_kernel<<<8192, 256, 0, stream>>>(feat, x1, x2);
-
-  for (int i = 0; i < 2; ++i) {
-    wconv_kernel<<<256, 256, 0, stream>>>(w_qk + i*65536, wtb + (i*5+0)*65536, 128, 512);
-    wconv_kernel<<<256, 256, 0, stream>>>(w_v  + i*65536, wtb + (i*5+1)*65536, 128, 512);
-    wconv_kernel<<<256, 256, 0, stream>>>(w_out+ i*65536, wtb + (i*5+2)*65536, 512, 128);
-    wconv_kernel<<<256, 256, 0, stream>>>(ffw1 + i*65536, wtb + (i*5+3)*65536, 128, 512);
-    wconv_kernel<<<256, 256, 0, stream>>>(ffw2 + i*65536, wtb + (i*5+4)*65536, 512, 128);
-  }
+  wconv_all<<<2560, 256, 0, stream>>>(w_qk, w_v, w_out, ffw1, ffw2, wtb);
 
   for (int i = 0; i < 2; ++i) {
     const unsigned short* Wqv = wtb + (i*5+0)*65536;
@@ -683,31 +695,30 @@
     const unsigned short* W1  = wtb + (i*5+3)*65536;
     const unsigned short* W2  = wtb + (i*5+4)*65536;
 
-    ln_kernel<<<4096, 256, 0, stream>>>(x2, nullptr, ln1g + i*128, ln1b + i*128,
-                                        xmb, 16384, 2048, 2176, 1);
-    memfill_kernel<<<512, 256, 0, stream>>>(memkv + i*16384, xmb);
+    ln_kernel<<<4352, 256, 0, stream>>>(x2, nullptr, ln1g + i*128, ln1b + i*128,
+                                        xmb, 16384, 2048, 2176, 1,
+                                        memkv + i*16384, 1024);
 
     gemm_qv<<<dim3(16, 272), 256, 0, stream>>>(xmb, Wqv, qkb, vbb);
     norm_kernel<<<544, 256, 0, stream>>>(qkb, nrm);
 
-    local_attn_mfma<<<544, 128, 0, stream>>>(qkb, vbb, nrm, opart, lpart);
-    local_comb<<<1088, 256, 0, stream>>>(opart, lpart, aob);
-
     hash_kernel<<<408, 256, 0, stream>>>(qkb, rots + i*4352, bkt);
     sort_kernel<<<192, 256, 0, stream>>>(bkt, st);
-    lsh_attn_mfma<<<3264, 128, 0, stream>>>(qkb, vbb, nrm, st, oall, logi);
-    comb_kernel<<<3264, 256, 0, stream>>>(oall, logi, aob);
+
+    fused_attn<<<3808, 128, 0, stream>>>(qkb, vbb, nrm, st, oall, logi, opart, lpart);
+
+    comb_fused<<<4352, 256, 0, stream>>>(oall, logi, opart, lpart, aob);
 
     gemm_bf16<<<dim3(2, 256), 256, 0, stream>>>(aob, Wo, b_out + i*128, x1, x1, nullptr,
                                                 16384, 128, 512, 2048, 2176, 0);
     ln_kernel<<<4096, 256, 0, stream>>>(x1, nullptr, ln2g + i*128, ln2b + i*128,
-                                        xmb, 16384, 1, 1, 1);
+                                        xmb, 16384, 1, 1, 1, nullptr, 0);
     gemm_bf16<<<dim3(8, 256), 256, 0, stream>>>(xmb, W1, ffb1 + i*512, nullptr, nullptr, hb,
                                                 16384, 512, 128, 1, 1, 1);
     gemm_bf16<<<dim3(2, 256), 256, 0, stream>>>(hb, W2, ffb2 + i*128, x2, x2, nullptr,
                                                 16384, 128, 512, 1, 1, 0);
   }
 
-  ln_kernel<<<4096, 256, 0, stream>>>(x1, x2, lnfg, lnfb, xm, 16384, 1, 1, 0);
+  ln_kernel<<<4096, 256, 0, stream>>>(x1, x2, lnfg, lnfb, xm, 16384, 1, 1, 0, nullptr, 0);
   pool_kernel<<<1024, 256, 0, stream>>>(xm, outp);
 }
```
